# Performance work log

Measured on AMD Instinct MI355X. Metric: run time of the kernel, lower is better.

## Reference

```python
import jax, jax.numpy as jnp
import numpy as np

D_MODEL = 1024
N_HEADS = 16
D_K = 64
D_FF = 4096
B = 8
S = 1024
NEG = -1e32
EPS = 1e-5


def _layer_norm(x, g, b):
    mu = jnp.mean(x, axis=-1, keepdims=True)
    var = jnp.var(x, axis=-1, keepdims=True)
    return (x - mu) * jax.lax.rsqrt(var + EPS) * g + b


def setup_inputs() -> dict:
    key = jax.random.key(0)
    ks = jax.random.split(key, 16)
    sc = 0.02
    inp = {
        'x': jax.random.normal(ks[0], (B, S, D_MODEL), dtype=jnp.float32),
        'Wq': jax.random.normal(ks[1], (D_MODEL, D_MODEL), jnp.float32) * sc,
        'bq': jnp.zeros((D_MODEL,), jnp.float32),
        'Wk': jax.random.normal(ks[2], (D_MODEL, D_MODEL), jnp.float32) * sc,
        'bk': jnp.zeros((D_MODEL,), jnp.float32),
        'Wv': jax.random.normal(ks[3], (D_MODEL, D_MODEL), jnp.float32) * sc,
        'bv': jnp.zeros((D_MODEL,), jnp.float32),
        'Wo': jax.random.normal(ks[4], (D_MODEL, D_MODEL), jnp.float32) * sc,
        'bo': jnp.zeros((D_MODEL,), jnp.float32),
        'W1': jax.random.normal(ks[5], (D_MODEL, D_FF), jnp.float32) * sc,
        'b1': jnp.zeros((D_FF,), jnp.float32),
        'W2': jax.random.normal(ks[6], (D_FF, D_MODEL), jnp.float32) * sc,
        'b2': jnp.zeros((D_MODEL,), jnp.float32),
        'g1': jnp.ones((D_MODEL,), jnp.float32),
        'beta1': jnp.zeros((D_MODEL,), jnp.float32),
        'g3': jnp.ones((D_MODEL,), jnp.float32),
        'beta3': jnp.zeros((D_MODEL,), jnp.float32),
    }
    return inp


def _block(x, Wq, bq, Wk, bk, Wv, bv, Wo, bo, W1, b1, W2, b2, g1, beta1, g3, beta3):
    bs, seqlen, _ = x.shape
    # QKV projections -> [b, h, s, d_k]
    def split_heads(t):
        return t.reshape(bs, seqlen, N_HEADS, D_K).transpose(0, 2, 1, 3)
    q = split_heads(x @ Wq + bq)
    k = split_heads(x @ Wk + bk)
    v = split_heads(x @ Wv + bv)
    # scores [b,h,s,s]
    scores = jnp.einsum('bhqd,bhkd->bhqk', q, k) / jnp.sqrt(jnp.float32(D_K))
    # mask=0 case: src_mask = (triu(ones, k=0) == 0) -> allow strictly lower (j < i)
    i = jnp.arange(seqlen)[:, None]
    j = jnp.arange(seqlen)[None, :]
    allowed = (j < i)  # [s, s]
    scores = jnp.where(allowed[None, None], scores, NEG)
    attn = jax.nn.softmax(scores, axis=-1)
    # zero_pad: zero out the first query row of attention probs
    attn = attn * (i > 0).astype(attn.dtype)[None, None]
    ctx = jnp.einsum('bhqk,bhkd->bhqd', attn, v)  # [b,h,s,d_k]
    concat = ctx.transpose(0, 2, 1, 3).reshape(bs, seqlen, D_MODEL)
    attn_out = concat @ Wo + bo
    # residual + LN (dropout p=0)
    h1 = _layer_norm(x + attn_out, g1, beta1)
    # position-wise FFN
    ffn = jax.nn.relu(h1 @ W1 + b1) @ W2 + b2
    out = _layer_norm(h1 + ffn, g3, beta3)
    return out


def reference(x, Wq, bq, Wk, bk, Wv, bv, Wo, bo, W1, b1, W2, b2, g1, beta1, g3, beta3):
    return _block(x, Wq, bq, Wk, bk, Wv, bv, Wo, bo, W1, b1, W2, b2, g1, beta1, g3, beta3)
```

## Files before the change

### kernel.cpp

```cpp
#include <hip/hip_runtime.h>
#include <hip/hip_bf16.h>

typedef __bf16 bf16x8 __attribute__((ext_vector_type(8)));
typedef __bf16 bf16x4 __attribute__((ext_vector_type(4)));
typedef float f32x4 __attribute__((ext_vector_type(4)));

#define GLOBAL_LOAD_LDS16(gp, lp)                                              \
  __builtin_amdgcn_global_load_lds(                                            \
      (const __attribute__((address_space(1))) void*)(gp),                     \
      (__attribute__((address_space(3))) void*)(lp), 16, 0, 0)

__global__ __launch_bounds__(256) void transpose4_f2b_k(
    const float* __restrict__ s0, const float* __restrict__ s1,
    const float* __restrict__ s2, const float* __restrict__ s3,
    __bf16* __restrict__ dst) {
  __shared__ float tile[32][33];
  const float* srcs[4] = {s0, s1, s2, s3};
  const float* src = srcs[blockIdx.z];
  __bf16* d = dst + ((size_t)blockIdx.z << 20);
  const int bx = blockIdx.x * 32, by = blockIdx.y * 32;
  const int tx = threadIdx.x & 31, ty = threadIdx.x >> 5;
#pragma unroll
  for (int i = 0; i < 32; i += 8)
    tile[ty + i][tx] = src[(size_t)(by + ty + i) * 1024 + bx + tx];
  __syncthreads();
#pragma unroll
  for (int i = 0; i < 32; i += 8)
    d[(size_t)(bx + ty + i) * 1024 + by + tx] = (__bf16)tile[tx][ty + i];
}

__global__ __launch_bounds__(256) void transpose_f2b_k(
    const float* __restrict__ src, __bf16* __restrict__ dst, int R, int C) {
  __shared__ float tile[32][33];
  const int bx = blockIdx.x * 32, by = blockIdx.y * 32;
  const int tx = threadIdx.x & 31, ty = threadIdx.x >> 5;
#pragma unroll
  for (int i = 0; i < 32; i += 8)
    tile[ty + i][tx] = src[(size_t)(by + ty + i) * C + bx + tx];
  __syncthreads();
#pragma unroll
  for (int i = 0; i < 32; i += 8)
    dst[(size_t)(bx + ty + i) * R + by + tx] = (__bf16)tile[tx][ty + i];
}

__global__ __launch_bounds__(256) void transpose_v_k(
    const __bf16* __restrict__ src, __bf16* __restrict__ dst) {
  __shared__ __bf16 tile[32][33];
  const int bh = blockIdx.z;
  const int s0 = blockIdx.x * 32, d0 = blockIdx.y * 32;
  const size_t base = (size_t)bh << 16;
  const int tx = threadIdx.x & 31, ty = threadIdx.x >> 5;
#pragma unroll
  for (int i = 0; i < 32; i += 8)
    tile[ty + i][tx] = src[base + (size_t)(s0 + ty + i) * 64 + d0 + tx];
  __syncthreads();
#pragma unroll
  for (int i = 0; i < 32; i += 8)
    dst[base + (size_t)(d0 + ty + i) * 1024 + s0 + tx] = tile[tx][ty + i];
}

__global__ __launch_bounds__(256) void convert_f2b_k(const float* __restrict__ s,
                                                     __bf16* __restrict__ d) {
  const size_t i = ((size_t)blockIdx.x * 256 + threadIdx.x) * 4;
  const float4 v = *(const float4*)(s + i);
  bf16x4 o;
  o[0] = (__bf16)v.x; o[1] = (__bf16)v.y; o[2] = (__bf16)v.z; o[3] = (__bf16)v.w;
  *(bf16x4*)(d + i) = o;
}

__global__ void concat3_k(const float* a, const float* b, const float* c,
                          float* o) {
  int i = blockIdx.x * 256 + threadIdx.x;
  if (i < 1024) o[i] = a[i];
  else if (i < 2048) o[i] = b[i - 1024];
  else if (i < 3072) o[i] = c[i - 2048];
}

#define STG(P, rowbase, Kld, kbase, DST)                                       \
  do {                                                                         \
    GLOBAL_LOAD_LDS16((P) + (size_t)((rowbase) + wave * 16 + srow) * (Kld) +   \
                          (kbase) + sch8,                                      \
                      (DST) + wave * 1024);                                    \
    GLOBAL_LOAD_LDS16((P) + (size_t)((rowbase) + wave * 16 + 8 + srow) *       \
                              (Kld) + (kbase) + sch8,                          \
                      (DST) + wave * 1024 + 512);                              \
  } while (0)

template <int EPI>
__global__ __launch_bounds__(256, 2) void gemm_db(const __bf16* __restrict__ A,
                                                  const __bf16* __restrict__ Bt,
                                                  const float* __restrict__ bias,
                                                  __bf16* __restrict__ C,
                                                  int M, int N, int K) {
  __shared__ __align__(16) __bf16 Abuf[2][128 * 64];
  __shared__ __align__(16) __bf16 Bbuf[2][128 * 64];
  const int tid = threadIdx.x;
  const int wave = tid >> 6, lane = tid & 63;
  const int quad = lane >> 4, l15 = lane & 15;
  const int wm = wave >> 1, wn = wave & 1;

  const int nwg = gridDim.x;
  const int cpx = nwg >> 3;
  const int bid = blockIdx.x;
  const int wg = (bid & 7) * cpx + (bid >> 3);
  const int gy = N >> 7;
  const int tm = wg / gy, tn = wg - tm * gy;
  const int m0 = tm << 7, n0 = tn << 7;

  const int srow = lane >> 3;
  const int sch8 = ((lane & 7) ^ srow) * 8;
  const int aoff = (wm * 64 + l15) * 64;
  const int boff = (wn * 64 + l15) * 64;
  const int c0 = (quad ^ (l15 & 7)) * 8;

  bf16x8 af[4][2], bfr[4][2];
  f32x4 acc[4][4] = {};

  const int NT = K >> 6;

  const __bf16* a_c = Abuf[0];
  const __bf16* a_n = Abuf[1];
  const __bf16* b_c = Bbuf[0];
  const __bf16* b_n = Bbuf[1];

  STG(A, m0, K, 0, (__bf16*)a_c);
  STG(A, m0 + 64, K, 0, (__bf16*)a_c + 64 * 64);
  STG(Bt, n0, K, 0, (__bf16*)b_c);
  STG(Bt, n0 + 64, K, 0, (__bf16*)b_c + 64 * 64);
  asm volatile("s_waitcnt vmcnt(0)" ::: "memory");
  __builtin_amdgcn_s_barrier();
  asm volatile("" ::: "memory");

  for (int t = 0; t < NT; ++t) {
#pragma unroll
    for (int f = 0; f < 4; ++f) {
      af[f][0] = *(const bf16x8*)(a_c + aoff + f * 1024 + c0);
      af[f][1] = *(const bf16x8*)(a_c + aoff + f * 1024 + (c0 ^ 32));
    }
#pragma unroll
    for (int g = 0; g < 4; ++g) {
      bfr[g][0] = *(const bf16x8*)(b_c + boff + g * 1024 + c0);
      bfr[g][1] = *(const bf16x8*)(b_c + boff + g * 1024 + (c0 ^ 32));
    }
    const int kn = (t + 1) << 6;
    const bool pf = (t + 1 < NT);
    if (pf) {
      STG(A, m0, K, kn, (__bf16*)a_n);
      STG(A, m0 + 64, K, kn, (__bf16*)a_n + 64 * 64);
      STG(Bt, n0, K, kn, (__bf16*)b_n);
      STG(Bt, n0 + 64, K, kn, (__bf16*)b_n + 64 * 64);
    }
    __builtin_amdgcn_s_setprio(1);
#pragma unroll
    for (int f = 0; f < 4; ++f)
#pragma unroll
      for (int g = 0; g < 4; ++g) {
        acc[f][g] = __builtin_amdgcn_mfma_f32_16x16x32_bf16(
            af[f][0], bfr[g][0], acc[f][g], 0, 0, 0);
        acc[f][g] = __builtin_amdgcn_mfma_f32_16x16x32_bf16(
            af[f][1], bfr[g][1], acc[f][g], 0, 0, 0);
      }
    __builtin_amdgcn_s_setprio(0);
    if (pf) {
      asm volatile("s_waitcnt vmcnt(0)" ::: "memory");
      __builtin_amdgcn_s_barrier();
      asm volatile("" ::: "memory");
    }
    const __bf16* ta = a_c; a_c = a_n; a_n = ta;
    const __bf16* tb = b_c; b_c = b_n; b_n = tb;
  }

  float bvv[4];
#pragma unroll
  for (int g = 0; g < 4; ++g) bvv[g] = bias[n0 + wn * 64 + g * 16 + l15];
#pragma unroll
  for (int f = 0; f < 4; ++f)
#pragma unroll
    for (int i = 0; i < 4; ++i) {
      const int row = m0 + wm * 64 + f * 16 + quad * 4 + i;
#pragma unroll
      for (int g = 0; g < 4; ++g) {
        const int col = n0 + wn * 64 + g * 16 + l15;
        float v = acc[f][g][i] + bvv[g];
        if (EPI == 1) v = fmaxf(v, 0.0f);
        size_t oidx;
        if (EPI == 2) {
          const int which = col >> 10, wi = col & 1023;
          const int h = wi >> 6, d = wi & 63;
          const int b = row >> 10, s = row & 1023;
          oidx = ((size_t)which << 23) +
                 (((size_t)(b * 16 + h) << 16) + s * 64 + d);
        } else {
          oidx = (size_t)row * N + col;
        }
        C[oidx] = (__bf16)v;
      }
    }
}

__global__ __launch_bounds__(256) void attn_kernel(const __bf16* __restrict__ Q,
                                                   const __bf16* __restrict__ Kg,
                                                   const __bf16* __restrict__ Vt,
                                                   __bf16* __restrict__ ctx) {
  const int qp = blockIdx.x;
  const int bh = blockIdx.y;
  const int b = bh >> 4, h = bh & 15;
  const int tid = threadIdx.x, wave = tid >> 6, lane = tid & 63;
  const int quad = lane >> 4, l15 = lane & 15;
  const size_t hoff = (size_t)bh << 16;
  const __bf16* Qh = Q + hoff;
  const __bf16* Kh = Kg + hoff;
  const __bf16* Vh = Vt + hoff;

  __shared__ __align__(16) __bf16 Ks[64 * 64];
  __shared__ __align__(16) __bf16 Vs[64 * 64];
  __shared__ __align__(16) __bf16 Ps[4][32 * 72];
  __shared__ float lL[128];

  const int skey = wave * 8 + (lane >> 3);
  const int sgr = lane & 7;

#pragma unroll
  for (int pass = 0; pass < 2; ++pass) {
    const int qt = pass ? (7 - qp) : qp;
    const int qb = qt * 128;

    bf16x8 qf[2][2];
#pragma unroll
    for (int g = 0; g < 2; ++g) {
      const int qrow = qb + wave * 32 + g * 16 + l15;
      bf16x8 t0 = *(const bf16x8*)(Qh + (size_t)qrow * 64 + quad * 8);
      bf16x8 t1 = *(const bf16x8*)(Qh + (size_t)qrow * 64 + 32 + quad * 8);
#pragma unroll
      for (int e = 0; e < 8; ++e) {
        qf[g][0][e] = (__bf16)((float)t0[e] * 0.125f);
        qf[g][1][e] = (__bf16)((float)t1[e] * 0.125f);
      }
    }

    f32x4 oacc[4][2] = {};
    float lrun[2][4] = {};

    const int ktmax = 2 * qt + 1;
    for (int kt = 0; kt <= ktmax; ++kt) {
      __syncthreads();
#pragma unroll
      for (int j = 0; j < 2; ++j) {
        const int row = skey + 32 * j;
        GLOBAL_LOAD_LDS16(
            Kh + (size_t)(kt * 64 + row) * 64 + ((sgr ^ (row & 7)) * 8),
            Ks + j * 2048 + wave * 512);
        GLOBAL_LOAD_LDS16(
            Vh + (size_t)row * 1024 + kt * 64 + ((sgr ^ (row & 7)) * 8),
            Vs + j * 2048 + wave * 512);
      }
      __syncthreads();

      f32x4 sacc[2][4] = {};
#pragma unroll
      for (int nt = 0; nt < 4; ++nt) {
        const int key = nt * 16 + l15, sw = key & 7;
        bf16x8 kf0 = *(const bf16x8*)(Ks + key * 64 + ((quad ^ sw) * 8));
        bf16x8 kf1 = *(const bf16x8*)(Ks + key * 64 + (((quad + 4) ^ sw) * 8));
#pragma unroll
        for (int g = 0; g < 2; ++g) {
          sacc[g][nt] = __builtin_amdgcn_mfma_f32_16x16x32_bf16(
              qf[g][0], kf0, sacc[g][nt], 0, 0, 0);
          sacc[g][nt] = __builtin_amdgcn_mfma_f32_16x16x32_bf16(
              qf[g][1], kf1, sacc[g][nt], 0, 0, 0);
        }
      }

      const bool tilemask = (kt >= 2 * qt);
#pragma unroll
      for (int g = 0; g < 2; ++g)
#pragma unroll
        for (int nt = 0; nt < 4; ++nt) {
          const int key = kt * 64 + nt * 16 + l15;
#pragma unroll
          for (int r = 0; r < 4; ++r) {
            float p = __expf(fminf(sacc[g][nt][r], 60.0f));
            if (tilemask && key >= qb + wave * 32 + g * 16 + quad * 4 + r)
              p = 0.0f;
            sacc[g][nt][r] = p;
            lrun[g][r] += p;
          }
        }

#pragma unroll
      for (int g = 0; g < 2; ++g)
#pragma unroll
        for (int nt = 0; nt < 4; ++nt)
#pragma unroll
          for (int r = 0; r < 4; ++r)
            Ps[wave][(g * 16 + quad * 4 + r) * 72 + nt * 16 + l15] =
                (__bf16)sacc[g][nt][r];

#pragma unroll
      for (int kc = 0; kc < 2; ++kc) {
        bf16x8 pf[2];
#pragma unroll
        for (int g = 0; g < 2; ++g)
          pf[g] = *(const bf16x8*)(&Ps[wave][(g * 16 + l15) * 72 + kc * 32 +
                                             quad * 8]);
#pragma unroll
        for (int mdt = 0; mdt < 4; ++mdt) {
          const int d = mdt * 16 + l15, sw = d & 7;
          bf16x8 vf =
              *(const bf16x8*)(Vs + d * 64 + (((kc * 4 + quad) ^ sw) * 8));
#pragma unroll
          for (int g = 0; g < 2; ++g)
            oacc[mdt][g] = __builtin_amdgcn_mfma_f32_16x16x32_bf16(
                vf, pf[g], oacc[mdt][g], 0, 0, 0);
        }
      }
    }

#pragma unroll
    for (int g = 0; g < 2; ++g)
#pragma unroll
      for (int r = 0; r < 4; ++r) {
        float s = lrun[g][r];
#pragma unroll
        for (int d = 1; d < 16; d <<= 1) s += __shfl_xor(s, d);
        if (l15 == 0) lL[wave * 32 + g * 16 + quad * 4 + r] = s;
      }
    float linv[2];
#pragma unroll
    for (int g = 0; g < 2; ++g) {
      const float l = lL[wave * 32 + g * 16 + l15];
      linv[g] = (qb + wave * 32 + g * 16 + l15 == 0) ? 0.0f : (1.0f / l);
    }
    __bf16* Ot = Ps[wave];
#pragma unroll
    for (int mdt = 0; mdt < 4; ++mdt)
#pragma unroll
      for (int g = 0; g < 2; ++g)
#pragma unroll
        for (int r = 0; r < 4; ++r)
          Ot[(g * 16 + l15) * 72 + mdt * 16 + quad * 4 + r] =
              (__bf16)(oacc[mdt][g][r] * linv[g]);
#pragma unroll
    for (int rr = 0; rr < 2; ++rr)
#pragma unroll
      for (int j = 0; j < 2; ++j) {
        const int row = rr * 16 + (lane >> 2), chk = (lane & 3) + 4 * j;
        bf16x8 ov = *(const bf16x8*)(Ot + row * 72 + chk * 8);
        const size_t oi = ((size_t)(b * 1024 + qb + wave * 32 + row)) * 1024 +
                          h * 64 + chk * 8;
        *(bf16x8*)(ctx + oi) = ov;
      }
  }
}

template <typename TX, typename TY, typename TO>
__global__ __launch_bounds__(256) void add_ln_kernel(const TX* __restrict__ x,
                                                     const TY* __restrict__ y,
                                                     const float* __restrict__ g,
                                                     const float* __restrict__ be,
                                                     TO* __restrict__ out) {
  const int row = blockIdx.x;
  const size_t base = (size_t)row * 1024;
  const int t = threadIdx.x;
  float xv[4], yv[4];
  if constexpr (sizeof(TX) == 4) {
    const float4 a = *(const float4*)(x + base + t * 4);
    xv[0] = a.x; xv[1] = a.y; xv[2] = a.z; xv[3] = a.w;
  } else {
    const bf16x4 a = *(const bf16x4*)(x + base + t * 4);
#pragma unroll
    for (int i = 0; i < 4; ++i) xv[i] = (float)a[i];
  }
  if constexpr (sizeof(TY) == 4) {
    const float4 a = *(const float4*)(y + base + t * 4);
    yv[0] = a.x; yv[1] = a.y; yv[2] = a.z; yv[3] = a.w;
  } else {
    const bf16x4 a = *(const bf16x4*)(y + base + t * 4);
#pragma unroll
    for (int i = 0; i < 4; ++i) yv[i] = (float)a[i];
  }
  float v[4], s = 0.0f, s2 = 0.0f;
#pragma unroll
  for (int i = 0; i < 4; ++i) {
    v[i] = xv[i] + yv[i];
    s += v[i];
    s2 += v[i] * v[i];
  }
#pragma unroll
  for (int m = 1; m < 64; m <<= 1) {
    s += __shfl_xor(s, m);
    s2 += __shfl_xor(s2, m);
  }
  __shared__ float ss[4], ss2[4];
  const int w = t >> 6;
  if ((t & 63) == 0) { ss[w] = s; ss2[w] = s2; }
  __syncthreads();
  s = ss[0] + ss[1] + ss[2] + ss[3];
  s2 = ss2[0] + ss2[1] + ss2[2] + ss2[3];
  const float mu = s * (1.0f / 1024.0f);
  const float var = s2 * (1.0f / 1024.0f) - mu * mu;
  const float rstd = rsqrtf(var + 1e-5f);
#pragma unroll
  for (int i = 0; i < 4; ++i) {
    const float o = (v[i] - mu) * rstd * g[t * 4 + i] + be[t * 4 + i];
    out[base + t * 4 + i] = (TO)o;
  }
}

extern "C" void kernel_launch(void* const* d_in, const int* in_sizes, int n_in,
                              void* d_out, int out_size, void* d_ws,
                              size_t ws_size, hipStream_t stream) {
  (void)in_sizes; (void)n_in; (void)out_size; (void)ws_size;
  const float* x   = (const float*)d_in[0];
  const float* Wq  = (const float*)d_in[1];
  const float* bq  = (const float*)d_in[2];
  const float* Wk  = (const float*)d_in[3];
  const float* bk  = (const float*)d_in[4];
  const float* Wv  = (const float*)d_in[5];
  const float* bv  = (const float*)d_in[6];
  const float* Wo  = (const float*)d_in[7];
  const float* bo  = (const float*)d_in[8];
  const float* W1  = (const float*)d_in[9];
  const float* b1  = (const float*)d_in[10];
  const float* W2  = (const float*)d_in[11];
  const float* b2  = (const float*)d_in[12];
  const float* g1  = (const float*)d_in[13];
  const float* be1 = (const float*)d_in[14];
  const float* g3  = (const float*)d_in[15];
  const float* be3 = (const float*)d_in[16];

  char* ws = (char*)d_ws;
  __bf16* Qb    = (__bf16*)(ws + 0);
  __bf16* Kb    = (__bf16*)(ws + (16u << 20));
  __bf16* Vb    = (__bf16*)(ws + (32u << 20));
  __bf16* ctx   = (__bf16*)(ws + (48u << 20));
  __bf16* mid   = (__bf16*)(ws + 0);
  __bf16* aout  = (__bf16*)(ws + (64u << 20));
  __bf16* h1    = aout;
  __bf16* xb    = (__bf16*)(ws + (80u << 20));
  __bf16* Vtb   = (__bf16*)(ws + (80u << 20));
  __bf16* fout  = (__bf16*)(ws + (80u << 20));
  __bf16* WqkvT = (__bf16*)(ws + (96u << 20));
  __bf16* WoT   = (__bf16*)(ws + (96u << 20) + 3 * (1u << 21));
  __bf16* W1T   = (__bf16*)(ws + (104u << 20));
  __bf16* W2T   = (__bf16*)(ws + (112u << 20));
  float*  bqkv  = (float*)(ws + (120u << 20));
  float*  outp  = (float*)d_out;

  const dim3 blk(256);
  convert_f2b_k<<<dim3(8192), blk, 0, stream>>>(x, xb);
  transpose4_f2b_k<<<dim3(32, 32, 4), blk, 0, stream>>>(Wq, Wk, Wv, Wo, WqkvT);
  transpose_f2b_k<<<dim3(128, 32), blk, 0, stream>>>(W1, W1T, 1024, 4096);
  transpose_f2b_k<<<dim3(32, 128), blk, 0, stream>>>(W2, W2T, 4096, 1024);
  concat3_k<<<dim3(12), blk, 0, stream>>>(bq, bk, bv, bqkv);

  gemm_db<2><<<dim3(64 * 24), blk, 0, stream>>>(xb, WqkvT, bqkv, Qb,
                                                8192, 3072, 1024);
  transpose_v_k<<<dim3(32, 2, 128), blk, 0, stream>>>(Vb, Vtb);
  attn_kernel<<<dim3(4, 128), blk, 0, stream>>>(Qb, Kb, Vtb, ctx);
  gemm_db<0><<<dim3(64 * 8), blk, 0, stream>>>(ctx, WoT, bo, aout,
                                               8192, 1024, 1024);
  add_ln_kernel<float, __bf16, __bf16><<<dim3(8192), blk, 0, stream>>>(
      x, aout, g1, be1, h1);
  gemm_db<1><<<dim3(64 * 32), blk, 0, stream>>>(h1, W1T, b1, mid,
                                                8192, 4096, 1024);
  gemm_db<0><<<dim3(64 * 8), blk, 0, stream>>>(mid, W2T, b2, fout,
                                               8192, 1024, 4096);
  add_ln_kernel<__bf16, __bf16, float><<<dim3(8192), blk, 0, stream>>>(
      h1, fout, g3, be3, outp);
}
```

Baseline: 461.5 us.

## Enlarge GEMM tiles to 256-row blocks with split-K LDS fragment loading

Replaces the 128x128 double-buffered GEMM with a templated kernel using 256-row M tiles and either 128- or 256-wide N tiles (4 or 8 waves). Each wave now computes a 128x64 sub-tile, raising arithmetic intensity per LDS and global load. Fragment loads are split into two k-halves interleaved with the MFMA batches, which lowers register pressure. The costs are more LDS per block, occupancy limited to one block per CU, and fewer blocks in the grid (256 for the N=1024 GEMMs), which could underfill the GPU's CUs.

```diff
diff --git a/kernel.cpp b/kernel.cpp
--- a/kernel.cpp
+++ b/kernel.cpp
@@ -86,35 +86,34 @@
                       (DST) + wave * 1024 + 512);                              \
   } while (0)
 
-template <int EPI>
-__global__ __launch_bounds__(256, 2) void gemm_db(const __bf16* __restrict__ A,
-                                                  const __bf16* __restrict__ Bt,
-                                                  const float* __restrict__ bias,
-                                                  __bf16* __restrict__ C,
-                                                  int M, int N, int K) {
-  __shared__ __align__(16) __bf16 Abuf[2][128 * 64];
-  __shared__ __align__(16) __bf16 Bbuf[2][128 * 64];
+template <int EPI, int NW, int BN>
+__global__ __launch_bounds__(NW * 64, 1) void gemm_w128(
+    const __bf16* __restrict__ A, const __bf16* __restrict__ Bt,
+    const float* __restrict__ bias, __bf16* __restrict__ C,
+    int M, int N, int K) {
+  __shared__ __align__(16) __bf16 Abuf[2][256 * 64];
+  __shared__ __align__(16) __bf16 Bbuf[2][BN * 64];
   const int tid = threadIdx.x;
   const int wave = tid >> 6, lane = tid & 63;
   const int quad = lane >> 4, l15 = lane & 15;
-  const int wm = wave >> 1, wn = wave & 1;
+  const int NWN = BN / 64;
+  const int wm = wave / NWN, wn = wave % NWN;
 
   const int nwg = gridDim.x;
   const int cpx = nwg >> 3;
   const int bid = blockIdx.x;
   const int wg = (bid & 7) * cpx + (bid >> 3);
-  const int gy = N >> 7;
+  const int gy = N / BN;
   const int tm = wg / gy, tn = wg - tm * gy;
-  const int m0 = tm << 7, n0 = tn << 7;
+  const int m0 = tm << 8, n0 = tn * BN;
 
   const int srow = lane >> 3;
   const int sch8 = ((lane & 7) ^ srow) * 8;
-  const int aoff = (wm * 64 + l15) * 64;
+  const int aoff = (wm * 128 + l15) * 64;
   const int boff = (wn * 64 + l15) * 64;
   const int c0 = (quad ^ (l15 & 7)) * 8;
 
-  bf16x8 af[4][2], bfr[4][2];
-  f32x4 acc[4][4] = {};
+  f32x4 acc[8][4] = {};
 
   const int NT = K >> 6;
 
@@ -123,43 +122,55 @@
   const __bf16* b_c = Bbuf[0];
   const __bf16* b_n = Bbuf[1];
 
-  STG(A, m0, K, 0, (__bf16*)a_c);
-  STG(A, m0 + 64, K, 0, (__bf16*)a_c + 64 * 64);
-  STG(Bt, n0, K, 0, (__bf16*)b_c);
-  STG(Bt, n0 + 64, K, 0, (__bf16*)b_c + 64 * 64);
+#pragma unroll
+  for (int p = 0; p < 256 / (NW * 16); ++p)
+    STG(A, m0 + p * NW * 16, K, 0, (__bf16*)a_c + p * NW * 1024);
+#pragma unroll
+  for (int p = 0; p < BN / (NW * 16); ++p)
+    STG(Bt, n0 + p * NW * 16, K, 0, (__bf16*)b_c + p * NW * 1024);
   asm volatile("s_waitcnt vmcnt(0)" ::: "memory");
   __builtin_amdgcn_s_barrier();
   asm volatile("" ::: "memory");
 
   for (int t = 0; t < NT; ++t) {
-#pragma unroll
-    for (int f = 0; f < 4; ++f) {
-      af[f][0] = *(const bf16x8*)(a_c + aoff + f * 1024 + c0);
-      af[f][1] = *(const bf16x8*)(a_c + aoff + f * 1024 + (c0 ^ 32));
-    }
-#pragma unroll
-    for (int g = 0; g < 4; ++g) {
-      bfr[g][0] = *(const bf16x8*)(b_c + boff + g * 1024 + c0);
-      bfr[g][1] = *(const bf16x8*)(b_c + boff + g * 1024 + (c0 ^ 32));
-    }
     const int kn = (t + 1) << 6;
     const bool pf = (t + 1 < NT);
     if (pf) {
-      STG(A, m0, K, kn, (__bf16*)a_n);
-      STG(A, m0 + 64, K, kn, (__bf16*)a_n + 64 * 64);
-      STG(Bt, n0, K, kn, (__bf16*)b_n);
-      STG(Bt, n0 + 64, K, kn, (__bf16*)b_n + 64 * 64);
-    }
+#pragma unroll
+      for (int p = 0; p < 256 / (NW * 16); ++p)
+        STG(A, m0 + p * NW * 16, K, kn, (__bf16*)a_n + p * NW * 1024);
+#pragma unroll
+      for (int p = 0; p < BN / (NW * 16); ++p)
+        STG(Bt, n0 + p * NW * 16, K, kn, (__bf16*)b_n + p * NW * 1024);
+    }
+    bf16x8 af[8], bfr[4];
+#pragma unroll
+    for (int f = 0; f < 8; ++f)
+      af[f] = *(const bf16x8*)(a_c + aoff + f * 1024 + c0);
+#pragma unroll
+    for (int g = 0; g < 4; ++g)
+      bfr[g] = *(const bf16x8*)(b_c + boff + g * 1024 + c0);
     __builtin_amdgcn_s_setprio(1);
 #pragma unroll
-    for (int f = 0; f < 4; ++f)
-#pragma unroll
-      for (int g = 0; g < 4; ++g) {
+    for (int f = 0; f < 8; ++f)
+#pragma unroll
+      for (int g = 0; g < 4; ++g)
         acc[f][g] = __builtin_amdgcn_mfma_f32_16x16x32_bf16(
-            af[f][0], bfr[g][0], acc[f][g], 0, 0, 0);
+            af[f], bfr[g], acc[f][g], 0, 0, 0);
+    __builtin_amdgcn_s_setprio(0);
+#pragma unroll
+    for (int f = 0; f < 8; ++f)
+      af[f] = *(const bf16x8*)(a_c + aoff + f * 1024 + (c0 ^ 32));
+#pragma unroll
+    for (int g = 0; g < 4; ++g)
+      bfr[g] = *(const bf16x8*)(b_c + boff + g * 1024 + (c0 ^ 32));
+    __builtin_amdgcn_s_setprio(1);
+#pragma unroll
+    for (int f = 0; f < 8; ++f)
+#pragma unroll
+      for (int g = 0; g < 4; ++g)
         acc[f][g] = __builtin_amdgcn_mfma_f32_16x16x32_bf16(
-            af[f][1], bfr[g][1], acc[f][g], 0, 0, 0);
-      }
+            af[f], bfr[g], acc[f][g], 0, 0, 0);
     __builtin_amdgcn_s_setprio(0);
     if (pf) {
       asm volatile("s_waitcnt vmcnt(0)" ::: "memory");
@@ -174,10 +185,10 @@
 #pragma unroll
   for (int g = 0; g < 4; ++g) bvv[g] = bias[n0 + wn * 64 + g * 16 + l15];
 #pragma unroll
-  for (int f = 0; f < 4; ++f)
+  for (int f = 0; f < 8; ++f)
 #pragma unroll
     for (int i = 0; i < 4; ++i) {
-      const int row = m0 + wm * 64 + f * 16 + quad * 4 + i;
+      const int row = m0 + wm * 128 + f * 16 + quad * 4 + i;
 #pragma unroll
       for (int g = 0; g < 4; ++g) {
         const int col = n0 + wn * 64 + g * 16 + l15;
@@ -448,24 +459,25 @@
   float*  outp  = (float*)d_out;
 
   const dim3 blk(256);
+  const dim3 blk512(512);
   convert_f2b_k<<<dim3(8192), blk, 0, stream>>>(x, xb);
   transpose4_f2b_k<<<dim3(32, 32, 4), blk, 0, stream>>>(Wq, Wk, Wv, Wo, WqkvT);
   transpose_f2b_k<<<dim3(128, 32), blk, 0, stream>>>(W1, W1T, 1024, 4096);
   transpose_f2b_k<<<dim3(32, 128), blk, 0, stream>>>(W2, W2T, 4096, 1024);
   concat3_k<<<dim3(12), blk, 0, stream>>>(bq, bk, bv, bqkv);
 
-  gemm_db<2><<<dim3(64 * 24), blk, 0, stream>>>(xb, WqkvT, bqkv, Qb,
-                                                8192, 3072, 1024);
+  gemm_w128<2, 4, 128><<<dim3(768), blk, 0, stream>>>(xb, WqkvT, bqkv, Qb,
+                                                      8192, 3072, 1024);
   transpose_v_k<<<dim3(32, 2, 128), blk, 0, stream>>>(Vb, Vtb);
   attn_kernel<<<dim3(4, 128), blk, 0, stream>>>(Qb, Kb, Vtb, ctx);
-  gemm_db<0><<<dim3(64 * 8), blk, 0, stream>>>(ctx, WoT, bo, aout,
-                                               8192, 1024, 1024);
+  gemm_w128<0, 4, 128><<<dim3(256), blk, 0, stream>>>(ctx, WoT, bo, aout,
+                                                      8192, 1024, 1024);
   add_ln_kernel<float, __bf16, __bf16><<<dim3(8192), blk, 0, stream>>>(
       x, aout, g1, be1, h1);
-  gemm_db<1><<<dim3(64 * 32), blk, 0, stream>>>(h1, W1T, b1, mid,
-                                                8192, 4096, 1024);
-  gemm_db<0><<<dim3(64 * 8), blk, 0, stream>>>(mid, W2T, b2, fout,
-                                               8192, 1024, 4096);
+  gemm_w128<1, 8, 256><<<dim3(512), blk512, 0, stream>>>(h1, W1T, b1, mid,
+                                                         8192, 4096, 1024);
+  gemm_w128<0, 4, 128><<<dim3(256), blk, 0, stream>>>(mid, W2T, b2, fout,
+                                                      8192, 1024, 4096);
   add_ln_kernel<__bf16, __bf16, float><<<dim3(8192), blk, 0, stream>>>(
       h1, fout, g3, be3, outp);
 }
```

After: 529.1 us. 1.15x slower.
